# Optimization experiments

Hardware: AMD Instinct MI355X
Metric: run time of the kernel (lower is better)

The kernel has to match this reference:

```python
import jax, jax.numpy as jnp
import numpy as np

N_NODES = 100000
N_EDGES = 800000
IN_FEATS = 64
HIDDEN = 128
OUT_FEATS = 64
BN_EPS = 1e-5


def setup_inputs() -> dict:
    key = jax.random.key(0)
    ks = jax.random.split(key, 10)
    x = jax.random.normal(ks[0], (N_NODES, IN_FEATS), dtype=jnp.float32)
    edge_src = jax.random.randint(ks[1], (N_EDGES,), 0, N_NODES, dtype=jnp.int64)
    edge_dst = jax.random.randint(ks[2], (N_EDGES,), 0, N_NODES, dtype=jnp.int64)
    def lin(k, fan_in, fan_out):
        return jax.random.normal(k, (fan_in, fan_out), dtype=jnp.float32) / np.sqrt(fan_in)
    return {
        "x": x,
        "edge_src": edge_src,
        "edge_dst": edge_dst,
        "W_self1": lin(ks[3], IN_FEATS, HIDDEN),
        "W_neigh1": lin(ks[4], IN_FEATS, HIDDEN),
        "b1": jnp.zeros((HIDDEN,), jnp.float32),
        "bn_gamma": jnp.ones((HIDDEN,), jnp.float32),
        "bn_beta": jnp.zeros((HIDDEN,), jnp.float32),
        "W_self2": lin(ks[5], HIDDEN, OUT_FEATS),
        "W_neigh2": lin(ks[6], HIDDEN, OUT_FEATS),
        "b2": jnp.zeros((OUT_FEATS,), jnp.float32),
    }


def _sage_mean(h, edge_src, edge_dst, W_self, W_neigh, b, n_nodes):
    # mean aggregation over in-edges (SpMM): gather src feats, segment-sum by dst
    msg = h[edge_src]                                              # [E, F]
    summed = jax.ops.segment_sum(msg, edge_dst, num_segments=n_nodes)
    deg = jax.ops.segment_sum(jnp.ones(edge_dst.shape, h.dtype), edge_dst,
                              num_segments=n_nodes)
    agg = summed / jnp.maximum(deg, 1.0)[:, None]                  # zero-degree -> 0
    return h @ W_self + agg @ W_neigh + b


def reference(x, edge_src, edge_dst, W_self1, W_neigh1, b1, bn_gamma, bn_beta,
              W_self2, W_neigh2, b2):
    n = x.shape[0]
    h = _sage_mean(x, edge_src, edge_dst, W_self1, W_neigh1, b1, n)   # [N, hidden]
    # BatchNorm1d over the node dimension (training-mode batch stats)
    mu = jnp.mean(h, axis=0)
    var = jnp.var(h, axis=0)
    h = bn_gamma * (h - mu) * jax.lax.rsqrt(var + BN_EPS) + bn_beta
    h = jax.nn.relu(h)                                                # dropout = identity (eval)
    return _sage_mean(h, edge_src, edge_dst, W_self2, W_neigh2, b2, n)
```

## Files before the change

kernel.cpp:

```cpp
#include <hip/hip_runtime.h>

#define N_NODES 100000
#define N_EDGES 800000
#define IN_F 64
#define HID 128
#define OUT_F 64
#define BN_EPS 1e-5f
#define SCAN_NBLK ((N_NODES + 255) / 256)

typedef __attribute__((ext_vector_type(8))) short short8v;
typedef __attribute__((ext_vector_type(4))) float f32x4;

static __device__ __forceinline__ unsigned short f2bf(float f) {
  unsigned u = __float_as_uint(f);
  return (unsigned short)((u + 0x7FFFu + ((u >> 16) & 1u)) >> 16);
}
static __device__ __forceinline__ float bflo(unsigned u) {
  return __uint_as_float(u << 16);
}
static __device__ __forceinline__ float bfhi(unsigned u) {
  return __uint_as_float(u & 0xFFFF0000u);
}

__global__ __launch_bounds__(256) void cvtzero_kernel(
    const float* __restrict__ x, unsigned short* __restrict__ xb,
    int* __restrict__ cursor) {
  int t = blockIdx.x * 256 + threadIdx.x;
  if (t < N_NODES / 4) {
    int4 z = {0, 0, 0, 0};
    reinterpret_cast<int4*>(cursor)[t] = z;
  }
  if (t >= N_NODES * IN_F / 8) return;
  float4 a = reinterpret_cast<const float4*>(x)[t * 2];
  float4 b = reinterpret_cast<const float4*>(x)[t * 2 + 1];
  uint4 o;
  o.x = (unsigned)f2bf(a.x) | ((unsigned)f2bf(a.y) << 16);
  o.y = (unsigned)f2bf(a.z) | ((unsigned)f2bf(a.w) << 16);
  o.z = (unsigned)f2bf(b.x) | ((unsigned)f2bf(b.y) << 16);
  o.w = (unsigned)f2bf(b.z) | ((unsigned)f2bf(b.w) << 16);
  reinterpret_cast<uint4*>(xb)[t] = o;
}

__global__ __launch_bounds__(256) void pass1_kernel(
    const int* __restrict__ edst, int* __restrict__ cursor,
    unsigned short* __restrict__ pos16) {
  int t = blockIdx.x * 256 + threadIdx.x;
  if (t >= N_EDGES / 4) return;
  int4 d = reinterpret_cast<const int4*>(edst)[t];
  ushort4 p;
  p.x = (unsigned short)atomicAdd(cursor + d.x, 1);
  p.y = (unsigned short)atomicAdd(cursor + d.y, 1);
  p.z = (unsigned short)atomicAdd(cursor + d.z, 1);
  p.w = (unsigned short)atomicAdd(cursor + d.w, 1);
  reinterpret_cast<ushort4*>(pos16)[t] = p;
}

__global__ __launch_bounds__(256) void blocksum_kernel(
    const int* __restrict__ degi, int* __restrict__ bsum) {
  __shared__ int ls[256];
  int i = blockIdx.x * 256 + threadIdx.x;
  ls[threadIdx.x] = (i < N_NODES) ? degi[i] : 0;
  __syncthreads();
  for (int off = 128; off > 0; off >>= 1) {
    if (threadIdx.x < off) ls[threadIdx.x] += ls[threadIdx.x + off];
    __syncthreads();
  }
  if (threadIdx.x == 0) bsum[blockIdx.x] = ls[0];
}

__global__ __launch_bounds__(512) void scanb_kernel(
    const int* __restrict__ bsum, int* __restrict__ boff,
    int* __restrict__ rowstart, float* __restrict__ bnsum) {
  __shared__ int ls[512];
  int t = threadIdx.x;
  if (t < 256) bnsum[t] = 0.f;
  int v = (t < SCAN_NBLK) ? bsum[t] : 0;
  ls[t] = v;
  __syncthreads();
  for (int off = 1; off < 512; off <<= 1) {
    int u = (t >= off) ? ls[t - off] : 0;
    __syncthreads();
    ls[t] += u;
    __syncthreads();
  }
  if (t < SCAN_NBLK) boff[t] = ls[t] - v;
  if (t == 511) rowstart[N_NODES] = ls[511];
}

__global__ __launch_bounds__(256) void writerow_kernel(
    const int* __restrict__ degi, const int* __restrict__ boff,
    int* __restrict__ rowstart) {
  __shared__ int ls[256];
  int i = blockIdx.x * 256 + threadIdx.x;
  int t = threadIdx.x;
  int v = (i < N_NODES) ? degi[i] : 0;
  ls[t] = v;
  __syncthreads();
  for (int off = 1; off < 256; off <<= 1) {
    int u = (t >= off) ? ls[t - off] : 0;
    __syncthreads();
    ls[t] += u;
    __syncthreads();
  }
  if (i < N_NODES) rowstart[i] = boff[blockIdx.x] + ls[t] - v;
}

__global__ __launch_bounds__(256) void scatter_kernel(
    const int* __restrict__ esrc, const int* __restrict__ edst,
    const unsigned short* __restrict__ pos16,
    const int* __restrict__ rowstart, int* __restrict__ csr) {
  int t = blockIdx.x * 256 + threadIdx.x;
  if (t >= N_EDGES / 4) return;
  int4 s = reinterpret_cast<const int4*>(esrc)[t];
  int4 d = reinterpret_cast<const int4*>(edst)[t];
  ushort4 p = reinterpret_cast<const ushort4*>(pos16)[t];
  csr[rowstart[d.x] + p.x] = s.x;
  csr[rowstart[d.y] + p.y] = s.y;
  csr[rowstart[d.z] + p.z] = s.z;
  csr[rowstart[d.w] + p.w] = s.w;
}

__global__ __launch_bounds__(256) void aggb1_kernel(
    const unsigned short* __restrict__ featb, const int* __restrict__ rowstart,
    const int* __restrict__ csr, unsigned short* __restrict__ dstb) {
  int n = blockIdx.x * 32 + (threadIdx.x >> 3);
  int j = threadIdx.x & 7;
  if (n >= N_NODES) return;
  int r0 = rowstart[n];
  int r1 = rowstart[n + 1];
  float acc[8] = {0.f, 0.f, 0.f, 0.f, 0.f, 0.f, 0.f, 0.f};
  int i = r0;
  for (; i + 3 < r1; i += 4) {
    int s0 = csr[i], s1 = csr[i + 1], s2 = csr[i + 2], s3 = csr[i + 3];
    uint4 v0 = *reinterpret_cast<const uint4*>(featb + (size_t)s0 * 64 + j * 8);
    uint4 v1 = *reinterpret_cast<const uint4*>(featb + (size_t)s1 * 64 + j * 8);
    uint4 v2 = *reinterpret_cast<const uint4*>(featb + (size_t)s2 * 64 + j * 8);
    uint4 v3 = *reinterpret_cast<const uint4*>(featb + (size_t)s3 * 64 + j * 8);
    acc[0] += (bflo(v0.x) + bflo(v1.x)) + (bflo(v2.x) + bflo(v3.x));
    acc[1] += (bfhi(v0.x) + bfhi(v1.x)) + (bfhi(v2.x) + bfhi(v3.x));
    acc[2] += (bflo(v0.y) + bflo(v1.y)) + (bflo(v2.y) + bflo(v3.y));
    acc[3] += (bfhi(v0.y) + bfhi(v1.y)) + (bfhi(v2.y) + bfhi(v3.y));
    acc[4] += (bflo(v0.z) + bflo(v1.z)) + (bflo(v2.z) + bflo(v3.z));
    acc[5] += (bfhi(v0.z) + bfhi(v1.z)) + (bfhi(v2.z) + bfhi(v3.z));
    acc[6] += (bflo(v0.w) + bflo(v1.w)) + (bflo(v2.w) + bflo(v3.w));
    acc[7] += (bfhi(v0.w) + bfhi(v1.w)) + (bfhi(v2.w) + bfhi(v3.w));
  }
  for (; i < r1; ++i) {
    int s0 = csr[i];
    uint4 v0 = *reinterpret_cast<const uint4*>(featb + (size_t)s0 * 64 + j * 8);
    acc[0] += bflo(v0.x);
    acc[1] += bfhi(v0.x);
    acc[2] += bflo(v0.y);
    acc[3] += bfhi(v0.y);
    acc[4] += bflo(v0.z);
    acc[5] += bfhi(v0.z);
    acc[6] += bflo(v0.w);
    acc[7] += bfhi(v0.w);
  }
  int deg = r1 - r0;
  float rd = 1.0f / (float)(deg > 0 ? deg : 1);
  uint4 o;
  o.x = (unsigned)f2bf(acc[0] * rd) | ((unsigned)f2bf(acc[1] * rd) << 16);
  o.y = (unsigned)f2bf(acc[2] * rd) | ((unsigned)f2bf(acc[3] * rd) << 16);
  o.z = (unsigned)f2bf(acc[4] * rd) | ((unsigned)f2bf(acc[5] * rd) << 16);
  o.w = (unsigned)f2bf(acc[6] * rd) | ((unsigned)f2bf(acc[7] * rd) << 16);
  *reinterpret_cast<uint4*>(dstb + (size_t)n * 64 + j * 8) = o;
}

__global__ __launch_bounds__(256) void aggb2_kernel(
    const unsigned short* __restrict__ zb, const unsigned short* __restrict__ sb,
    const int* __restrict__ rowstart, const int* __restrict__ csr,
    float* __restrict__ out) {
  int n = blockIdx.x * 32 + (threadIdx.x >> 3);
  int j = threadIdx.x & 7;
  if (n >= N_NODES) return;
  int r0 = rowstart[n];
  int r1 = rowstart[n + 1];
  float acc[8] = {0.f, 0.f, 0.f, 0.f, 0.f, 0.f, 0.f, 0.f};
  int i = r0;
  for (; i + 3 < r1; i += 4) {
    int s0 = csr[i], s1 = csr[i + 1], s2 = csr[i + 2], s3 = csr[i + 3];
    uint4 v0 = *reinterpret_cast<const uint4*>(zb + (size_t)s0 * 64 + j * 8);
    uint4 v1 = *reinterpret_cast<const uint4*>(zb + (size_t)s1 * 64 + j * 8);
    uint4 v2 = *reinterpret_cast<const uint4*>(zb + (size_t)s2 * 64 + j * 8);
    uint4 v3 = *reinterpret_cast<const uint4*>(zb + (size_t)s3 * 64 + j * 8);
    acc[0] += (bflo(v0.x) + bflo(v1.x)) + (bflo(v2.x) + bflo(v3.x));
    acc[1] += (bfhi(v0.x) + bfhi(v1.x)) + (bfhi(v2.x) + bfhi(v3.x));
    acc[2] += (bflo(v0.y) + bflo(v1.y)) + (bflo(v2.y) + bflo(v3.y));
    acc[3] += (bfhi(v0.y) + bfhi(v1.y)) + (bfhi(v2.y) + bfhi(v3.y));
    acc[4] += (bflo(v0.z) + bflo(v1.z)) + (bflo(v2.z) + bflo(v3.z));
    acc[5] += (bfhi(v0.z) + bfhi(v1.z)) + (bfhi(v2.z) + bfhi(v3.z));
    acc[6] += (bflo(v0.w) + bflo(v1.w)) + (bflo(v2.w) + bflo(v3.w));
    acc[7] += (bfhi(v0.w) + bfhi(v1.w)) + (bfhi(v2.w) + bfhi(v3.w));
  }
  for (; i < r1; ++i) {
    int s0 = csr[i];
    uint4 v0 = *reinterpret_cast<const uint4*>(zb + (size_t)s0 * 64 + j * 8);
    acc[0] += bflo(v0.x);
    acc[1] += bfhi(v0.x);
    acc[2] += bflo(v0.y);
    acc[3] += bfhi(v0.y);
    acc[4] += bflo(v0.z);
    acc[5] += bfhi(v0.z);
    acc[6] += bflo(v0.w);
    acc[7] += bfhi(v0.w);
  }
  int deg = r1 - r0;
  float rd = 1.0f / (float)(deg > 0 ? deg : 1);
  uint4 sv = *reinterpret_cast<const uint4*>(sb + (size_t)n * 64 + j * 8);
  float* dp = out + (size_t)n * 64 + j * 8;
  __builtin_nontemporal_store(bflo(sv.x) + acc[0] * rd, dp + 0);
  __builtin_nontemporal_store(bfhi(sv.x) + acc[1] * rd, dp + 1);
  __builtin_nontemporal_store(bflo(sv.y) + acc[2] * rd, dp + 2);
  __builtin_nontemporal_store(bfhi(sv.y) + acc[3] * rd, dp + 3);
  __builtin_nontemporal_store(bflo(sv.z) + acc[4] * rd, dp + 4);
  __builtin_nontemporal_store(bfhi(sv.z) + acc[5] * rd, dp + 5);
  __builtin_nontemporal_store(bflo(sv.w) + acc[6] * rd, dp + 6);
  __builtin_nontemporal_store(bfhi(sv.w) + acc[7] * rd, dp + 7);
}

__global__ __launch_bounds__(512) void gemm1_mfma(
    const unsigned short* __restrict__ xb,
    const unsigned short* __restrict__ aggxb, const float* __restrict__ Ws,
    const float* __restrict__ Wn, const float* __restrict__ b,
    unsigned short* __restrict__ hb) {
  __shared__ __align__(16) unsigned short wt[128 * 128];
  __shared__ float bs[HID];
  int tid = threadIdx.x;
  for (int i = tid; i < 128 * 128; i += 512) {
    int k = i >> 7, j = i & 127;
    float v = (k < 64) ? Ws[k * HID + j] : Wn[(k - 64) * HID + j];
    int idx = (j << 7) | k;
    wt[idx ^ ((j & 15) << 3)] = f2bf(v);
  }
  if (tid < HID) bs[tid] = b[tid];
  __syncthreads();

  int wave = tid >> 6, lane = tid & 63;
  int m = lane & 15, kg = lane >> 4;
  int rbase = blockIdx.x * 128 + wave * 16;
  int rowa = rbase + m;
  if (rowa >= N_NODES) rowa = N_NODES - 1;

  short8v a[4];
#pragma unroll
  for (int kt = 0; kt < 4; ++kt) {
    int c0 = kt * 32 + kg * 8;
    const unsigned short* src = (c0 < 64)
                                    ? (xb + (size_t)rowa * 64 + c0)
                                    : (aggxb + (size_t)rowa * 64 + (c0 - 64));
    a[kt] = *reinterpret_cast<const short8v*>(src);
  }

  f32x4 acc[8];
#pragma unroll
  for (int nt = 0; nt < 8; ++nt) acc[nt] = (f32x4){0.f, 0.f, 0.f, 0.f};

#pragma unroll
  for (int nt = 0; nt < 8; ++nt) {
    int col = nt * 16 + m;
    int base = col << 7;
    int sw = (col & 15) << 3;
#pragma unroll
    for (int kt = 0; kt < 4; ++kt) {
      int idx = (base | (kt * 32 + kg * 8)) ^ sw;
      short8v bf = *reinterpret_cast<const short8v*>(&wt[idx]);
      acc[nt] = __builtin_amdgcn_mfma_f32_16x16x32_bf16(a[kt], bf, acc[nt], 0, 0, 0);
    }
  }

#pragma unroll
  for (int nt = 0; nt < 8; ++nt) {
    int col = nt * 16 + m;
    float bias = bs[col];
#pragma unroll
    for (int r = 0; r < 4; ++r) {
      int rr = rbase + kg * 4 + r;
      if (rr < N_NODES) hb[(size_t)rr * HID + col] = f2bf(acc[nt][r] + bias);
    }
  }
}

__global__ __launch_bounds__(256) void bnstats_kernel(
    const unsigned short* __restrict__ hb, float* __restrict__ bnsum) {
  int j = threadIdx.x & 15;
  int g = threadIdx.x >> 4;
  float s[8] = {0.f, 0.f, 0.f, 0.f, 0.f, 0.f, 0.f, 0.f};
  float q[8] = {0.f, 0.f, 0.f, 0.f, 0.f, 0.f, 0.f, 0.f};
  for (int r = blockIdx.x * 16 + g; r < N_NODES; r += gridDim.x * 16) {
    uint4 v = *reinterpret_cast<const uint4*>(hb + (size_t)r * HID + j * 8);
    float f0 = bflo(v.x), f1 = bfhi(v.x), f2 = bflo(v.y), f3 = bfhi(v.y);
    float f4 = bflo(v.z), f5 = bfhi(v.z), f6 = bflo(v.w), f7 = bfhi(v.w);
    s[0] += f0; q[0] += f0 * f0;
    s[1] += f1; q[1] += f1 * f1;
    s[2] += f2; q[2] += f2 * f2;
    s[3] += f3; q[3] += f3 * f3;
    s[4] += f4; q[4] += f4 * f4;
    s[5] += f5; q[5] += f5 * f5;
    s[6] += f6; q[6] += f6 * f6;
    s[7] += f7; q[7] += f7 * f7;
  }
  __shared__ float lss[256 * 8];
  __shared__ float lqq[256 * 8];
#pragma unroll
  for (int e = 0; e < 8; ++e) {
    lss[threadIdx.x * 8 + e] = s[e];
    lqq[threadIdx.x * 8 + e] = q[e];
  }
  __syncthreads();
  if (threadIdx.x < 128) {
    int f = threadIdx.x;
    int jj = f >> 3, e = f & 7;
    float S = 0.f, Q = 0.f;
#pragma unroll
    for (int gg = 0; gg < 16; ++gg) {
      S += lss[(gg * 16 + jj) * 8 + e];
      Q += lqq[(gg * 16 + jj) * 8 + e];
    }
    unsafeAtomicAdd(bnsum + f, S);
    unsafeAtomicAdd(bnsum + 128 + f, Q);
  }
}

__global__ __launch_bounds__(512) void gemm2_mfma(
    const unsigned short* __restrict__ hb, const float* __restrict__ bnsum,
    const float* __restrict__ gamma, const float* __restrict__ beta,
    const float* __restrict__ Wn, const float* __restrict__ Ws,
    const float* __restrict__ b, unsigned short* __restrict__ zb,
    unsigned short* __restrict__ sb) {
  __shared__ __align__(16) unsigned short wt[128 * 128];
  __shared__ float scs[HID];
  __shared__ float shs[HID];
  __shared__ float bz[OUT_F];
  int tid = threadIdx.x;
  for (int i = tid; i < 128 * 128; i += 512) {
    int k = i >> 7, j = i & 127;
    float v = (j < 64) ? Wn[k * OUT_F + j] : Ws[k * OUT_F + (j - 64)];
    int idx = (j << 7) | k;
    wt[idx ^ ((j & 15) << 3)] = f2bf(v);
  }
  if (tid < HID) {
    const float invn = 1.0f / (float)N_NODES;
    float mu = bnsum[tid] * invn;
    float var = bnsum[128 + tid] * invn - mu * mu;
    float sc = gamma[tid] * rsqrtf(var + BN_EPS);
    scs[tid] = sc;
    shs[tid] = beta[tid] - mu * sc;
  }
  if (tid < OUT_F) bz[tid] = b[tid];
  __syncthreads();

  int wave = tid >> 6, lane = tid & 63;
  int m = lane & 15, kg = lane >> 4;
  int rbase = blockIdx.x * 128 + wave * 16;
  int rowa = rbase + m;
  if (rowa >= N_NODES) rowa = N_NODES - 1;

  short8v a[4];
#pragma unroll
  for (int kt = 0; kt < 4; ++kt) {
    int c0 = kt * 32 + kg * 8;
    uint4 raw = *reinterpret_cast<const uint4*>(hb + (size_t)rowa * HID + c0);
    float4 sc0 = *reinterpret_cast<const float4*>(&scs[c0]);
    float4 sc1 = *reinterpret_cast<const float4*>(&scs[c0 + 4]);
    float4 sh0 = *reinterpret_cast<const float4*>(&shs[c0]);
    float4 sh1 = *reinterpret_cast<const float4*>(&shs[c0 + 4]);
    short8v av;
    av[0] = (short)f2bf(fmaxf(bflo(raw.x) * sc0.x + sh0.x, 0.f));
    av[1] = (short)f2bf(fmaxf(bfhi(raw.x) * sc0.y + sh0.y, 0.f));
    av[2] = (short)f2bf(fmaxf(bflo(raw.y) * sc0.z + sh0.z, 0.f));
    av[3] = (short)f2bf(fmaxf(bfhi(raw.y) * sc0.w + sh0.w, 0.f));
    av[4] = (short)f2bf(fmaxf(bflo(raw.z) * sc1.x + sh1.x, 0.f));
    av[5] = (short)f2bf(fmaxf(bfhi(raw.z) * sc1.y + sh1.y, 0.f));
    av[6] = (short)f2bf(fmaxf(bflo(raw.w) * sc1.z + sh1.z, 0.f));
    av[7] = (short)f2bf(fmaxf(bfhi(raw.w) * sc1.w + sh1.w, 0.f));
    a[kt] = av;
  }

  f32x4 acc[8];
#pragma unroll
  for (int nt = 0; nt < 8; ++nt) acc[nt] = (f32x4){0.f, 0.f, 0.f, 0.f};

#pragma unroll
  for (int nt = 0; nt < 8; ++nt) {
    int col = nt * 16 + m;
    int base = col << 7;
    int sw = (col & 15) << 3;
#pragma unroll
    for (int kt = 0; kt < 4; ++kt) {
      int idx = (base | (kt * 32 + kg * 8)) ^ sw;
      short8v bf = *reinterpret_cast<const short8v*>(&wt[idx]);
      acc[nt] = __builtin_amdgcn_mfma_f32_16x16x32_bf16(a[kt], bf, acc[nt], 0, 0, 0);
    }
  }

#pragma unroll
  for (int nt = 0; nt < 8; ++nt) {
    int col = nt * 16 + m;
#pragma unroll
    for (int r = 0; r < 4; ++r) {
      int rr = rbase + kg * 4 + r;
      if (rr < N_NODES) {
        float v = acc[nt][r];
        if (col < 64)
          zb[(size_t)rr * OUT_F + col] = f2bf(v);
        else
          sb[(size_t)rr * OUT_F + (col - 64)] = f2bf(v + bz[col - 64]);
      }
    }
  }
}

extern "C" void kernel_launch(void* const* d_in, const int* in_sizes, int n_in,
                              void* d_out, int out_size, void* d_ws,
                              size_t ws_size, hipStream_t stream) {
  const float* x = (const float*)d_in[0];
  const int* esrc = (const int*)d_in[1];
  const int* edst = (const int*)d_in[2];
  const float* Ws1 = (const float*)d_in[3];
  const float* Wn1 = (const float*)d_in[4];
  const float* b1 = (const float*)d_in[5];
  const float* gamma = (const float*)d_in[6];
  const float* beta = (const float*)d_in[7];
  const float* Ws2 = (const float*)d_in[8];
  const float* Wn2 = (const float*)d_in[9];
  const float* b2 = (const float*)d_in[10];
  float* out = (float*)d_out;

  float* ws = (float*)d_ws;
  float* bnsum = ws;
  int* cursor = (int*)(ws + 512);
  int* rowstart = cursor + N_NODES;
  int* bsum = rowstart + N_NODES + 1;
  int* boff = bsum + SCAN_NBLK;
  int* csr = boff + SCAN_NBLK;
  int pos16_off = ((512 + 2 * N_NODES + 1 + 2 * SCAN_NBLK + N_EDGES) + 3) & ~3;
  unsigned short* pos16 = (unsigned short*)(ws + pos16_off);
  unsigned short* xb = (unsigned short*)(ws + pos16_off + N_EDGES / 2);
  unsigned short* aggxb = xb + (size_t)N_NODES * 64;
  unsigned short* sb = aggxb + (size_t)N_NODES * 64;
  unsigned short* hb = sb + (size_t)N_NODES * 64;

  const int e4grid = (N_EDGES / 4 + 255) / 256;
  cvtzero_kernel<<<(N_NODES * IN_F / 8 + 255) / 256, 256, 0, stream>>>(x, xb,
                                                                       cursor);
  pass1_kernel<<<e4grid, 256, 0, stream>>>(edst, cursor, pos16);
  blocksum_kernel<<<SCAN_NBLK, 256, 0, stream>>>(cursor, bsum);
  scanb_kernel<<<1, 512, 0, stream>>>(bsum, boff, rowstart, bnsum);
  writerow_kernel<<<SCAN_NBLK, 256, 0, stream>>>(cursor, boff, rowstart);
  scatter_kernel<<<e4grid, 256, 0, stream>>>(esrc, edst, pos16, rowstart, csr);

  const int ggrid = (N_NODES + 127) / 128;
  const int agrid = (N_NODES + 31) / 32;
  aggb1_kernel<<<agrid, 256, 0, stream>>>(xb, rowstart, csr, aggxb);
  gemm1_mfma<<<ggrid, 512, 0, stream>>>(xb, aggxb, Ws1, Wn1, b1, hb);

  bnstats_kernel<<<256, 256, 0, stream>>>(hb, bnsum);

  gemm2_mfma<<<ggrid, 512, 0, stream>>>(hb, bnsum, gamma, beta, Wn2, Ws2, b2,
                                        aggxb, sb);
  aggb2_kernel<<<agrid, 256, 0, stream>>>(aggxb, sb, rowstart, csr, out);
}
```

Baseline: 178.7 us.

## Fuse layer-1 neighbor aggregation into the first GEMM kernel via shared memory

The separate layer-1 aggregation kernel is removed. Each 128-row GEMM block now gathers and averages its neighbors' bf16 features into an LDS tile, which feeds the MFMA A operand directly. This drops one kernel launch and the global write and re-read of the aggregated buffer. In exchange the gather runs 4 threads per node with 32-byte loads and 2-way unrolling instead of 8 threads with 4-way unrolling. It also adds LDS pressure, which may lower occupancy while latency-bound gathers are in flight.

```diff
diff --git a/kernel.cpp b/kernel.cpp
--- a/kernel.cpp
+++ b/kernel.cpp
@@ -120,51 +120,146 @@
   csr[rowstart[d.w] + p.w] = s.w;
 }
 
-__global__ __launch_bounds__(256) void aggb1_kernel(
-    const unsigned short* __restrict__ featb, const int* __restrict__ rowstart,
-    const int* __restrict__ csr, unsigned short* __restrict__ dstb) {
-  int n = blockIdx.x * 32 + (threadIdx.x >> 3);
-  int j = threadIdx.x & 7;
-  if (n >= N_NODES) return;
-  int r0 = rowstart[n];
-  int r1 = rowstart[n + 1];
-  float acc[8] = {0.f, 0.f, 0.f, 0.f, 0.f, 0.f, 0.f, 0.f};
-  int i = r0;
-  for (; i + 3 < r1; i += 4) {
-    int s0 = csr[i], s1 = csr[i + 1], s2 = csr[i + 2], s3 = csr[i + 3];
-    uint4 v0 = *reinterpret_cast<const uint4*>(featb + (size_t)s0 * 64 + j * 8);
-    uint4 v1 = *reinterpret_cast<const uint4*>(featb + (size_t)s1 * 64 + j * 8);
-    uint4 v2 = *reinterpret_cast<const uint4*>(featb + (size_t)s2 * 64 + j * 8);
-    uint4 v3 = *reinterpret_cast<const uint4*>(featb + (size_t)s3 * 64 + j * 8);
-    acc[0] += (bflo(v0.x) + bflo(v1.x)) + (bflo(v2.x) + bflo(v3.x));
-    acc[1] += (bfhi(v0.x) + bfhi(v1.x)) + (bfhi(v2.x) + bfhi(v3.x));
-    acc[2] += (bflo(v0.y) + bflo(v1.y)) + (bflo(v2.y) + bflo(v3.y));
-    acc[3] += (bfhi(v0.y) + bfhi(v1.y)) + (bfhi(v2.y) + bfhi(v3.y));
-    acc[4] += (bflo(v0.z) + bflo(v1.z)) + (bflo(v2.z) + bflo(v3.z));
-    acc[5] += (bfhi(v0.z) + bfhi(v1.z)) + (bfhi(v2.z) + bfhi(v3.z));
-    acc[6] += (bflo(v0.w) + bflo(v1.w)) + (bflo(v2.w) + bflo(v3.w));
-    acc[7] += (bfhi(v0.w) + bfhi(v1.w)) + (bfhi(v2.w) + bfhi(v3.w));
-  }
-  for (; i < r1; ++i) {
-    int s0 = csr[i];
-    uint4 v0 = *reinterpret_cast<const uint4*>(featb + (size_t)s0 * 64 + j * 8);
-    acc[0] += bflo(v0.x);
-    acc[1] += bfhi(v0.x);
-    acc[2] += bflo(v0.y);
-    acc[3] += bfhi(v0.y);
-    acc[4] += bflo(v0.z);
-    acc[5] += bfhi(v0.z);
-    acc[6] += bflo(v0.w);
-    acc[7] += bfhi(v0.w);
-  }
-  int deg = r1 - r0;
-  float rd = 1.0f / (float)(deg > 0 ? deg : 1);
-  uint4 o;
-  o.x = (unsigned)f2bf(acc[0] * rd) | ((unsigned)f2bf(acc[1] * rd) << 16);
-  o.y = (unsigned)f2bf(acc[2] * rd) | ((unsigned)f2bf(acc[3] * rd) << 16);
-  o.z = (unsigned)f2bf(acc[4] * rd) | ((unsigned)f2bf(acc[5] * rd) << 16);
-  o.w = (unsigned)f2bf(acc[6] * rd) | ((unsigned)f2bf(acc[7] * rd) << 16);
-  *reinterpret_cast<uint4*>(dstb + (size_t)n * 64 + j * 8) = o;
+__global__ __launch_bounds__(512) void gemm1_fused(
+    const unsigned short* __restrict__ xb, const int* __restrict__ rowstart,
+    const int* __restrict__ csr, const float* __restrict__ Ws,
+    const float* __restrict__ Wn, const float* __restrict__ b,
+    unsigned short* __restrict__ hb) {
+  __shared__ __align__(16) unsigned short wt[128 * 128];
+  __shared__ __align__(16) unsigned short aggl[128][72];
+  __shared__ float bs[HID];
+  int tid = threadIdx.x;
+  for (int i = tid; i < 128 * 128; i += 512) {
+    int k = i >> 7, j = i & 127;
+    float v = (k < 64) ? Ws[k * HID + j] : Wn[(k - 64) * HID + j];
+    int idx = (j << 7) | k;
+    wt[idx ^ ((j & 15) << 3)] = f2bf(v);
+  }
+  if (tid < HID) bs[tid] = b[tid];
+
+  {
+    int r_local = tid >> 2;
+    int jj = tid & 3;
+    int row = blockIdx.x * 128 + r_local;
+    float acc[16];
+#pragma unroll
+    for (int e = 0; e < 16; ++e) acc[e] = 0.f;
+    if (row < N_NODES) {
+      int r0 = rowstart[row];
+      int r1 = rowstart[row + 1];
+      int i = r0;
+      for (; i + 1 < r1; i += 2) {
+        int s0 = csr[i], s1 = csr[i + 1];
+        const uint4* p0 =
+            reinterpret_cast<const uint4*>(xb + (size_t)s0 * 64 + jj * 16);
+        const uint4* p1 =
+            reinterpret_cast<const uint4*>(xb + (size_t)s1 * 64 + jj * 16);
+        uint4 a0 = p0[0], b0 = p0[1];
+        uint4 a1 = p1[0], b1 = p1[1];
+        acc[0] += bflo(a0.x) + bflo(a1.x);
+        acc[1] += bfhi(a0.x) + bfhi(a1.x);
+        acc[2] += bflo(a0.y) + bflo(a1.y);
+        acc[3] += bfhi(a0.y) + bfhi(a1.y);
+        acc[4] += bflo(a0.z) + bflo(a1.z);
+        acc[5] += bfhi(a0.z) + bfhi(a1.z);
+        acc[6] += bflo(a0.w) + bflo(a1.w);
+        acc[7] += bfhi(a0.w) + bfhi(a1.w);
+        acc[8] += bflo(b0.x) + bflo(b1.x);
+        acc[9] += bfhi(b0.x) + bfhi(b1.x);
+        acc[10] += bflo(b0.y) + bflo(b1.y);
+        acc[11] += bfhi(b0.y) + bfhi(b1.y);
+        acc[12] += bflo(b0.z) + bflo(b1.z);
+        acc[13] += bfhi(b0.z) + bfhi(b1.z);
+        acc[14] += bflo(b0.w) + bflo(b1.w);
+        acc[15] += bfhi(b0.w) + bfhi(b1.w);
+      }
+      if (i < r1) {
+        int s0 = csr[i];
+        const uint4* p0 =
+            reinterpret_cast<const uint4*>(xb + (size_t)s0 * 64 + jj * 16);
+        uint4 a0 = p0[0], b0 = p0[1];
+        acc[0] += bflo(a0.x);
+        acc[1] += bfhi(a0.x);
+        acc[2] += bflo(a0.y);
+        acc[3] += bfhi(a0.y);
+        acc[4] += bflo(a0.z);
+        acc[5] += bfhi(a0.z);
+        acc[6] += bflo(a0.w);
+        acc[7] += bfhi(a0.w);
+        acc[8] += bflo(b0.x);
+        acc[9] += bfhi(b0.x);
+        acc[10] += bflo(b0.y);
+        acc[11] += bfhi(b0.y);
+        acc[12] += bflo(b0.z);
+        acc[13] += bfhi(b0.z);
+        acc[14] += bflo(b0.w);
+        acc[15] += bfhi(b0.w);
+      }
+      int deg = r1 - r0;
+      float rd = 1.0f / (float)(deg > 0 ? deg : 1);
+#pragma unroll
+      for (int e = 0; e < 16; ++e) acc[e] *= rd;
+    }
+    uint4 o0, o1;
+    o0.x = (unsigned)f2bf(acc[0]) | ((unsigned)f2bf(acc[1]) << 16);
+    o0.y = (unsigned)f2bf(acc[2]) | ((unsigned)f2bf(acc[3]) << 16);
+    o0.z = (unsigned)f2bf(acc[4]) | ((unsigned)f2bf(acc[5]) << 16);
+    o0.w = (unsigned)f2bf(acc[6]) | ((unsigned)f2bf(acc[7]) << 16);
+    o1.x = (unsigned)f2bf(acc[8]) | ((unsigned)f2bf(acc[9]) << 16);
+    o1.y = (unsigned)f2bf(acc[10]) | ((unsigned)f2bf(acc[11]) << 16);
+    o1.z = (unsigned)f2bf(acc[12]) | ((unsigned)f2bf(acc[13]) << 16);
+    o1.w = (unsigned)f2bf(acc[14]) | ((unsigned)f2bf(acc[15]) << 16);
+    uint4* dst = reinterpret_cast<uint4*>(&aggl[r_local][jj * 16]);
+    dst[0] = o0;
+    dst[1] = o1;
+  }
+  __syncthreads();
+
+  int wave = tid >> 6, lane = tid & 63;
+  int m = lane & 15, kg = lane >> 4;
+  int rbase = blockIdx.x * 128 + wave * 16;
+  int rowa = rbase + m;
+  if (rowa >= N_NODES) rowa = N_NODES - 1;
+  int lr = wave * 16 + m;
+
+  short8v a[4];
+#pragma unroll
+  for (int kt = 0; kt < 4; ++kt) {
+    int c0 = kt * 32 + kg * 8;
+    if (c0 < 64) {
+      a[kt] = *reinterpret_cast<const short8v*>(xb + (size_t)rowa * 64 + c0);
+    } else {
+      a[kt] = *reinterpret_cast<const short8v*>(&aggl[lr][c0 - 64]);
+    }
+  }
+
+  f32x4 acc[8];
+#pragma unroll
+  for (int nt = 0; nt < 8; ++nt) acc[nt] = (f32x4){0.f, 0.f, 0.f, 0.f};
+
+#pragma unroll
+  for (int nt = 0; nt < 8; ++nt) {
+    int col = nt * 16 + m;
+    int base = col << 7;
+    int sw = (col & 15) << 3;
+#pragma unroll
+    for (int kt = 0; kt < 4; ++kt) {
+      int idx = (base | (kt * 32 + kg * 8)) ^ sw;
+      short8v bf = *reinterpret_cast<const short8v*>(&wt[idx]);
+      acc[nt] = __builtin_amdgcn_mfma_f32_16x16x32_bf16(a[kt], bf, acc[nt], 0, 0, 0);
+    }
+  }
+
+#pragma unroll
+  for (int nt = 0; nt < 8; ++nt) {
+    int col = nt * 16 + m;
+    float bias = bs[col];
+#pragma unroll
+    for (int r = 0; r < 4; ++r) {
+      int rr = rbase + kg * 4 + r;
+      if (rr < N_NODES) hb[(size_t)rr * HID + col] = f2bf(acc[nt][r] + bias);
+    }
+  }
 }
 
 __global__ __launch_bounds__(256) void aggb2_kernel(
@@ -219,68 +314,6 @@
   __builtin_nontemporal_store(bfhi(sv.w) + acc[7] * rd, dp + 7);
 }
 
-__global__ __launch_bounds__(512) void gemm1_mfma(
-    const unsigned short* __restrict__ xb,
-    const unsigned short* __restrict__ aggxb, const float* __restrict__ Ws,
-    const float* __restrict__ Wn, const float* __restrict__ b,
-    unsigned short* __restrict__ hb) {
-  __shared__ __align__(16) unsigned short wt[128 * 128];
-  __shared__ float bs[HID];
-  int tid = threadIdx.x;
-  for (int i = tid; i < 128 * 128; i += 512) {
-    int k = i >> 7, j = i & 127;
-    float v = (k < 64) ? Ws[k * HID + j] : Wn[(k - 64) * HID + j];
-    int idx = (j << 7) | k;
-    wt[idx ^ ((j & 15) << 3)] = f2bf(v);
-  }
-  if (tid < HID) bs[tid] = b[tid];
-  __syncthreads();
-
-  int wave = tid >> 6, lane = tid & 63;
-  int m = lane & 15, kg = lane >> 4;
-  int rbase = blockIdx.x * 128 + wave * 16;
-  int rowa = rbase + m;
-  if (rowa >= N_NODES) rowa = N_NODES - 1;
-
-  short8v a[4];
-#pragma unroll
-  for (int kt = 0; kt < 4; ++kt) {
-    int c0 = kt * 32 + kg * 8;
-    const unsigned short* src = (c0 < 64)
-                                    ? (xb + (size_t)rowa * 64 + c0)
-                                    : (aggxb + (size_t)rowa * 64 + (c0 - 64));
-    a[kt] = *reinterpret_cast<const short8v*>(src);
-  }
-
-  f32x4 acc[8];
-#pragma unroll
-  for (int nt = 0; nt < 8; ++nt) acc[nt] = (f32x4){0.f, 0.f, 0.f, 0.f};
-
-#pragma unroll
-  for (int nt = 0; nt < 8; ++nt) {
-    int col = nt * 16 + m;
-    int base = col << 7;
-    int sw = (col & 15) << 3;
-#pragma unroll
-    for (int kt = 0; kt < 4; ++kt) {
-      int idx = (base | (kt * 32 + kg * 8)) ^ sw;
-      short8v bf = *reinterpret_cast<const short8v*>(&wt[idx]);
-      acc[nt] = __builtin_amdgcn_mfma_f32_16x16x32_bf16(a[kt], bf, acc[nt], 0, 0, 0);
-    }
-  }
-
-#pragma unroll
-  for (int nt = 0; nt < 8; ++nt) {
-    int col = nt * 16 + m;
-    float bias = bs[col];
-#pragma unroll
-    for (int r = 0; r < 4; ++r) {
-      int rr = rbase + kg * 4 + r;
-      if (rr < N_NODES) hb[(size_t)rr * HID + col] = f2bf(acc[nt][r] + bias);
-    }
-  }
-}
-
 __global__ __launch_bounds__(256) void bnstats_kernel(
     const unsigned short* __restrict__ hb, float* __restrict__ bnsum) {
   int j = threadIdx.x & 15;
@@ -437,8 +470,8 @@
   int pos16_off = ((512 + 2 * N_NODES + 1 + 2 * SCAN_NBLK + N_EDGES) + 3) & ~3;
   unsigned short* pos16 = (unsigned short*)(ws + pos16_off);
   unsigned short* xb = (unsigned short*)(ws + pos16_off + N_EDGES / 2);
-  unsigned short* aggxb = xb + (size_t)N_NODES * 64;
-  unsigned short* sb = aggxb + (size_t)N_NODES * 64;
+  unsigned short* zbuf = xb + (size_t)N_NODES * 64;
+  unsigned short* sb = zbuf + (size_t)N_NODES * 64;
   unsigned short* hb = sb + (size_t)N_NODES * 64;
 
   const int e4grid = (N_EDGES / 4 + 255) / 256;
@@ -452,12 +485,11 @@
 
   const int ggrid = (N_NODES + 127) / 128;
   const int agrid = (N_NODES + 31) / 32;
-  aggb1_kernel<<<agrid, 256, 0, stream>>>(xb, rowstart, csr, aggxb);
-  gemm1_mfma<<<ggrid, 512, 0, stream>>>(xb, aggxb, Ws1, Wn1, b1, hb);
+  gemm1_fused<<<ggrid, 512, 0, stream>>>(xb, rowstart, csr, Ws1, Wn1, b1, hb);
 
   bnstats_kernel<<<256, 256, 0, stream>>>(hb, bnsum);
 
   gemm2_mfma<<<ggrid, 512, 0, stream>>>(hb, bnsum, gamma, beta, Wn2, Ws2, b2,
-                                        aggxb, sb);
-  aggb2_kernel<<<agrid, 256, 0, stream>>>(aggxb, sb, rowstart, csr, out);
-}
+                                        zbuf, sb);
+  aggb2_kernel<<<agrid, 256, 0, stream>>>(zbuf, sb, rowstart, csr, out);
+}
```

Result: faster. 174.9 us, median of 2 (-2.1%).
